# Performance work log

Measured on AMD Instinct MI355X. Metric: run time of the kernel, lower is better.

Reference implementation:

```python
import jax, jax.numpy as jnp
import numpy as np

B, S, D = 2, 2048, 4096
H, KV, HD = 32, 8, 128
ROPE_BASE = 10000.0


def rotate_half(x):
    x1, x2 = jnp.split(x, 2, axis=-1)
    return jnp.concatenate((-x2, x1), axis=-1)


def rope_tables(seq_len, head_dim, position_ids):
    inv_freq = 1.0 / (ROPE_BASE ** (jnp.arange(0, head_dim, 2, dtype=jnp.float32) / head_dim))
    t = jnp.arange(seq_len, dtype=jnp.float32)
    freqs = t[:, None] * inv_freq[None, :]            # [S, HD/2]
    emb = jnp.concatenate((freqs, freqs), axis=-1)     # [S, HD]
    cos = jnp.cos(emb)[position_ids][:, None]          # [B, 1, S, HD]
    sin = jnp.sin(emb)[position_ids][:, None]
    return cos, sin


def setup_inputs() -> dict:
    key = jax.random.key(0)
    ks = jax.random.split(key, 5)
    sc = 0.02
    return {
        "hidden_states": jax.random.normal(ks[0], (B, S, D), jnp.float32),
        "Wq": jax.random.normal(ks[1], (H * HD, D), jnp.float32) * sc,
        "Wk": jax.random.normal(ks[2], (KV * HD, D), jnp.float32) * sc,
        "Wv": jax.random.normal(ks[3], (KV * HD, D), jnp.float32) * sc,
        "Wo": jax.random.normal(ks[4], (D, H * HD), jnp.float32) * sc,
        "position_ids": jnp.broadcast_to(jnp.arange(S, dtype=jnp.int32), (B, S)),
    }


def reference(hidden_states, Wq, Wk, Wv, Wo, position_ids):
    b, s, _ = hidden_states.shape
    n_rep = H // KV

    q = (hidden_states @ Wq.T).reshape(b, s, H, HD).transpose(0, 2, 1, 3)   # [B,H,S,HD]
    k = (hidden_states @ Wk.T).reshape(b, s, KV, HD).transpose(0, 2, 1, 3)  # [B,KV,S,HD]
    v = (hidden_states @ Wv.T).reshape(b, s, KV, HD).transpose(0, 2, 1, 3)

    cos, sin = rope_tables(s, HD, position_ids)
    q = q * cos + rotate_half(q) * sin
    k = k * cos + rotate_half(k) * sin

    # repeat_kv: [B,KV,S,HD] -> [B,H,S,HD]
    k = jnp.repeat(k, n_rep, axis=1)
    v = jnp.repeat(v, n_rep, axis=1)

    scores = jnp.einsum("bhqd,bhkd->bhqk", q, k) / jnp.sqrt(jnp.float32(HD))
    # causal additive mask (what the surrounding model always supplies)
    causal = jnp.tril(jnp.ones((s, s), dtype=bool))
    scores = jnp.where(causal[None, None], scores, jnp.finfo(jnp.float32).min)
    attn = jax.nn.softmax(scores.astype(jnp.float32), axis=-1).astype(q.dtype)

    out = jnp.einsum("bhqk,bhkd->bhqd", attn, v)        # [B,H,S,HD]
    out = out.transpose(0, 2, 1, 3).reshape(b, s, H * HD)
    return out @ Wo.T
```

## Files before the change

### kernel.cpp

```cpp
#include <hip/hip_runtime.h>
#include <stdint.h>
#include <math.h>

#define B_  2
#define S_  2048
#define D_  4096
#define H_  32
#define KV_ 8
#define HD_ 128
#define M_  (B_ * S_)

typedef unsigned short u16;
typedef unsigned int   u32;

__device__ __forceinline__ float bf2f(u16 u) {
  union { u32 i; float f; } x; x.i = ((u32)u) << 16; return x.f;
}
__device__ __forceinline__ u16 f2bf(float f) {
  union { float f; u32 i; } x; x.f = f;
  u32 r = x.i + 0x7fffu + ((x.i >> 16) & 1u);
  return (u16)(r >> 16);
}
__device__ __forceinline__ u32 pack_bf16_rh(float hi, float lo) {
  union { float f; u32 i; } a, c; a.f = hi; c.f = lo;
  return __builtin_amdgcn_perm(a.i + 0x8000u, c.i + 0x8000u, 0x07060302u);
}

typedef __attribute__((ext_vector_type(8))) short bf16x8;
typedef __attribute__((ext_vector_type(4))) float f32x4;

__device__ __forceinline__ void async_cp16(const void* g, void* l) {
  __builtin_amdgcn_global_load_lds(
      (const __attribute__((address_space(1))) u32*)g,
      (__attribute__((address_space(3))) u32*)l, 16, 0, 0);
}

#define SBAR   asm volatile("s_barrier" ::: "memory")
#define WAITL0 asm volatile("s_waitcnt lgkmcnt(0)" ::: "memory")
#define WAITV(n) asm volatile("s_waitcnt vmcnt(" #n ")" ::: "memory")

__global__ void k_f32_to_bf16(const float* __restrict__ src, u16* __restrict__ dst, int n) {
  int i = (blockIdx.x * 256 + threadIdx.x) * 4;
  if (i >= n) return;
  float4 v = *(const float4*)(src + i);
  ushort4 o;
  o.x = f2bf(v.x); o.y = f2bf(v.y); o.z = f2bf(v.z); o.w = f2bf(v.w);
  *(ushort4*)(dst + i) = o;
}

template <typename OutT>
__global__ __launch_bounds__(512, 2) void k_gemm256_bt(const u16* __restrict__ A,
                                                       const u16* __restrict__ Bm,
                                                       OutT* __restrict__ C,
                                                       int M, int N, int K) {
  __shared__ __align__(16) u16 As[2][256 * 64];
  __shared__ __align__(16) u16 Bs[2][256 * 64];
  const int t = threadIdx.x;
  const int l = t & 63;
  const int w = t >> 6;
  const int wr = w >> 2, wc = w & 3;
  const int quad = l >> 4, lm = l & 15, l7 = l & 7;
  const int m0 = blockIdx.y * 256, n0 = blockIdx.x * 256;

  const int srow = t >> 3;
  const int scb  = (t & 7) ^ (srow & 7);
  const u16* srcA = A  + (size_t)(m0 + srow) * K + scb * 8;
  const u16* srcB = Bm + (size_t)(n0 + srow) * K + scb * 8;
  u16* dA = &As[0][0] + t * 8;
  u16* dB = &Bs[0][0] + t * 8;
  const size_t row64 = (size_t)64 * K;

  const int rowA = (wr * 128 + lm) * 64;
  const int rowB = (wc * 64 + lm) * 64;
  const int kq0 = ((0 * 4 + quad) ^ l7) * 8;
  const int kq1 = ((1 * 4 + quad) ^ l7) * 8;
  const u16* As0 = &As[0][0];
  const u16* Bs0 = &Bs[0][0];

  f32x4 acc[8][4];
#pragma unroll
  for (int i2 = 0; i2 < 8; ++i2)
#pragma unroll
    for (int j2 = 0; j2 < 4; ++j2) {
      f32x4 z = {0.f, 0.f, 0.f, 0.f};
      acc[i2][j2] = z;
    }

  auto stgA = [&](int buf, int kt, int h) {
    const u16* s = srcA + (size_t)kt * 64 + (size_t)(h * 128) * K;
    u16* d = dA + buf * 16384 + h * 8192;
    async_cp16(s, d);
    async_cp16(s + row64, d + 4096);
  };
  auto stgB = [&](int buf, int kt, int h) {
    const u16* s = srcB + (size_t)kt * 64 + (size_t)(h * 128) * K;
    u16* d = dB + buf * 16384 + h * 8192;
    async_cp16(s, d);
    async_cp16(s + row64, d + 4096);
  };

  stgA(0, 0, 0); stgA(0, 0, 1);
  stgB(0, 0, 0); stgB(0, 0, 1);
  stgB(1, 1, 0); stgB(1, 1, 1);
  WAITV(4);
  SBAR;

  const int iters = K >> 7;
  for (int i = 0; i < iters; ++i) {
    const int kt = 2 * i;
    const bool notLast = (i + 1 < iters);
#pragma unroll
    for (int hf = 0; hf < 2; ++hf) {
      bf16x8 bfr[4][2];
#pragma unroll
      for (int q = 0; q < 4; ++q) {
        if (q == 0) {
#pragma unroll
          for (int fn = 0; fn < 4; ++fn) {
            const int ro = hf * 16384 + rowB + fn * 1024;
            bfr[fn][0] = *(const bf16x8*)&Bs0[ro + kq0];
            bfr[fn][1] = *(const bf16x8*)&Bs0[ro + kq1];
          }
        }
        bf16x8 af[2][2];
#pragma unroll
        for (int fo = 0; fo < 2; ++fo) {
          const int ro = hf * 16384 + rowA + (2 * q + fo) * 1024;
          af[fo][0] = *(const bf16x8*)&As0[ro + kq0];
          af[fo][1] = *(const bf16x8*)&As0[ro + kq1];
        }
        if (hf == 0) {
          if (q == 0)      stgA(1, kt + 1, 0);
          else if (q == 1) stgA(1, kt + 1, 1);
          else if (q == 2) { if (notLast) stgB(0, kt + 2, 0); }
          else {
            if (notLast) { stgB(0, kt + 2, 1); WAITV(4); }
            else WAITV(0);
          }
        } else if (notLast) {
          if (q == 0)      stgA(0, kt + 2, 0);
          else if (q == 1) stgA(0, kt + 2, 1);
          else if (q == 2) stgB(1, kt + 3, 0);
          else { stgB(1, kt + 3, 1); WAITV(4); }
        }
        SBAR;
        WAITL0;
        __builtin_amdgcn_s_setprio(1);
#pragma unroll
        for (int fo = 0; fo < 2; ++fo)
#pragma unroll
          for (int fn = 0; fn < 4; ++fn)
            acc[2 * q + fo][fn] = __builtin_amdgcn_mfma_f32_16x16x32_bf16(
                af[fo][0], bfr[fn][0], acc[2 * q + fo][fn], 0, 0, 0);
#pragma unroll
        for (int fo = 0; fo < 2; ++fo)
#pragma unroll
          for (int fn = 0; fn < 4; ++fn)
            acc[2 * q + fo][fn] = __builtin_amdgcn_mfma_f32_16x16x32_bf16(
                af[fo][1], bfr[fn][1], acc[2 * q + fo][fn], 0, 0, 0);
        __builtin_amdgcn_s_setprio(0);
        SBAR;
      }
    }
  }

#pragma unroll
  for (int fm = 0; fm < 8; ++fm) {
    const int row = m0 + wr * 128 + fm * 16 + quad * 4;
#pragma unroll
    for (int fn = 0; fn < 4; ++fn) {
      const int col = n0 + wc * 64 + fn * 16 + lm;
#pragma unroll
      for (int r = 0; r < 4; ++r) {
        float v = acc[fm][fn][r];
        if constexpr (sizeof(OutT) == 2)
          C[(size_t)(row + r) * N + col] = (OutT)f2bf(v);
        else
          C[(size_t)(row + r) * N + col] = v;
      }
    }
  }
}

__global__ __launch_bounds__(256) void k_rope(u16* __restrict__ Q, u16* __restrict__ Km,
                                              const int* __restrict__ pos_ids) {
  const int t = threadIdx.x;
  const int bs = blockIdx.x * 4 + (t >> 6);
  const int d = t & 63;
  const int hg = blockIdx.y;
  const float pos = (float)pos_ids[bs];
  const float ang = pos * expf(-(float)d * 0.1439115683121279f);
  float sn, cs;
  sincosf(ang, &sn, &cs);
#pragma unroll
  for (int j = 0; j < 4; j++) {
    const int hh = hg * 4 + j;
    u16* p = (hh < H_) ? (Q + (size_t)bs * (H_ * HD_) + hh * HD_)
                       : (Km + (size_t)bs * 2048 + (hh - H_) * HD_);
    const float x1 = bf2f(p[d]);
    const float x2 = bf2f(p[d + 64]);
    p[d]      = f2bf(x1 * cs - x2 * sn);
    p[d + 64] = f2bf(x2 * cs + x1 * sn);
  }
}

__global__ __launch_bounds__(256) void k_transpose_v(const u16* __restrict__ KVb,
                                                     u16* __restrict__ Vt) {
  __shared__ u16 tile[64][136];
  const int s0 = blockIdx.x * 64;
  const int kvh = blockIdx.y & 7, b = blockIdx.y >> 3;
  const int t = threadIdx.x;
  const int sl = t >> 2, d0 = (t & 3) * 32;
  const u16* src = KVb + (size_t)(b * S_ + s0 + sl) * 2048 + 1024 + kvh * 128 + d0;
#pragma unroll
  for (int j = 0; j < 4; j++)
    *(uint4*)&tile[sl][d0 + j * 8] = *(const uint4*)(src + j * 8);
  __syncthreads();
  const int lt = t & 63, wv = t >> 6;
  u16* dst = Vt + ((size_t)(b * KV_ + kvh) * HD_) * (size_t)S_ + s0 + lt;
#pragma unroll
  for (int i = 0; i < 32; i++) {
    const int d = i * 4 + wv;
    dst[(size_t)d * S_] = tile[lt][d];
  }
}

__global__ __launch_bounds__(256, 2) void k_attn_mfma(const u16* __restrict__ Q,
                                                      const u16* __restrict__ KVb,
                                                      const u16* __restrict__ Vt,
                                                      u16* __restrict__ O) {
  __shared__ __align__(16) u16 Ks[2][64 * 128];
  __shared__ __align__(16) u16 Vs[2][128 * 64];
  __shared__ __align__(16) u16 Ps[128 * 64];
  const int qt = (S_ / 128 - 1) - blockIdx.x;
  const int h = blockIdx.y, b = blockIdx.z;
  const int kvh = h >> 2;
  const int t = threadIdx.x;
  const int w = t >> 6, l = t & 63;
  const int quad = l >> 4, lm = l & 15, l7 = l & 7;
  const int q0 = qt * 128, wq = w * 32;

  bf16x8 qf[2][4];
#pragma unroll
  for (int nt = 0; nt < 2; nt++)
#pragma unroll
    for (int ks = 0; ks < 4; ks++) {
      const int qrow = q0 + wq + nt * 16 + lm;
      qf[nt][ks] = *(const bf16x8*)(Q + (size_t)(b * S_ + qrow) * (H_ * HD_)
                                    + h * HD_ + ks * 32 + quad * 8);
    }

  const u16* kSrc[4]; const u16* vSrc[4];
  int dstOff[4];
#pragma unroll
  for (int j = 0; j < 4; j++) {
    const int c = w * 4 + j;
    kSrc[j] = KVb + (size_t)(b * S_ + c * 4 + (l >> 4)) * 2048 + kvh * 128
              + 8 * ((l & 15) ^ ((c & 1) * 4 + (l >> 4)));
    vSrc[j] = Vt + ((size_t)(b * KV_ + kvh) * HD_ + c * 8 + (l >> 3)) * (size_t)S_
              + 8 * ((l & 7) ^ (l >> 3));
    dstOff[j] = c * 512 + l * 8;
  }

  f32x4 Oa[8][2];
#pragma unroll
  for (int dt = 0; dt < 8; dt++)
#pragma unroll
    for (int nt = 0; nt < 2; nt++) {
      f32x4 z = {0.f, 0.f, 0.f, 0.f};
      Oa[dt][nt] = z;
    }
  float lsum[2] = {0.f, 0.f};

  const int nTiles = (qt + 1) * 2;

#pragma unroll
  for (int j = 0; j < 4; j++) {
    async_cp16(kSrc[j], &Ks[0][dstOff[j]]);
    async_cp16(vSrc[j], &Vs[0][dstOff[j]]);
  }

  for (int tile = 0; tile < nTiles; tile++) {
    const int cur = tile & 1;
    __builtin_amdgcn_s_waitcnt(0);
    __syncthreads();
    if (tile + 1 < nTiles) {
      const size_t kAdv = (size_t)(tile + 1) * 64 * 2048;
      const int vAdv = (tile + 1) * 64;
      const int nxt = cur ^ 1;
#pragma unroll
      for (int j = 0; j < 4; j++) {
        async_cp16(kSrc[j] + kAdv, &Ks[nxt][dstOff[j]]);
        async_cp16(vSrc[j] + vAdv, &Vs[nxt][dstOff[j]]);
      }
    }
    const u16* KsC = Ks[cur];
    const u16* VsC = Vs[cur];

    f32x4 st[4][2];
#pragma unroll
    for (int kvt = 0; kvt < 4; kvt++)
#pragma unroll
      for (int nt = 0; nt < 2; nt++) {
        f32x4 z = {0.f, 0.f, 0.f, 0.f};
        st[kvt][nt] = z;
      }
#pragma unroll
    for (int ks = 0; ks < 4; ks++) {
      bf16x8 kf[4];
#pragma unroll
      for (int kvt = 0; kvt < 4; kvt++)
        kf[kvt] = *(const bf16x8*)&KsC[(kvt * 16 + lm) * 128 + ((ks * 4 + quad) ^ l7) * 8];
#pragma unroll
      for (int kvt = 0; kvt < 4; kvt++) {
        st[kvt][0] = __builtin_amdgcn_mfma_f32_16x16x32_bf16(kf[kvt], qf[0][ks], st[kvt][0], 0, 0, 0);
        st[kvt][1] = __builtin_amdgcn_mfma_f32_16x16x32_bf16(kf[kvt], qf[1][ks], st[kvt][1], 0, 0, 0);
      }
    }

    const int kt0 = tile * 64;
    const bool diag = (tile >= nTiles - 2);
#pragma unroll
    for (int nt = 0; nt < 2; nt++) {
      const int qg = q0 + wq + nt * 16 + lm;
      const int prow = (wq + nt * 16 + lm) * 64;
#pragma unroll
      for (int kvt = 0; kvt < 4; kvt++) {
        float p[4];
#pragma unroll
        for (int r = 0; r < 4; r++) {
          float e = __expf(st[kvt][nt][r] * 0.08838834764831845f);
          if (diag) {
            const int kg = kt0 + kvt * 16 + quad * 4 + r;
            e = (kg <= qg) ? e : 0.f;
          }
          p[r] = e;
          lsum[nt] += e;
        }
        uint2 pk;
        pk.x = pack_bf16_rh(p[1], p[0]);
        pk.y = pack_bf16_rh(p[3], p[2]);
        const int pb = (2 * kvt + (quad >> 1)) ^ l7;
        *(uint2*)&Ps[prow + pb * 8 + (quad & 1) * 4] = pk;
      }
    }

#pragma unroll
    for (int ks2 = 0; ks2 < 2; ks2++) {
      const int pboff = ((ks2 * 4 + quad) ^ l7) * 8;
      bf16x8 pf0 = *(const bf16x8*)&Ps[(wq + lm) * 64 + pboff];
      bf16x8 pf1 = *(const bf16x8*)&Ps[(wq + 16 + lm) * 64 + pboff];
#pragma unroll
      for (int dt = 0; dt < 8; dt++) {
        bf16x8 vf = *(const bf16x8*)&VsC[(dt * 16 + lm) * 64 + pboff];
        Oa[dt][0] = __builtin_amdgcn_mfma_f32_16x16x32_bf16(vf, pf0, Oa[dt][0], 0, 0, 0);
        Oa[dt][1] = __builtin_amdgcn_mfma_f32_16x16x32_bf16(vf, pf1, Oa[dt][1], 0, 0, 0);
      }
    }
  }

#pragma unroll
  for (int nt = 0; nt < 2; nt++) {
    lsum[nt] += __shfl_xor(lsum[nt], 16);
    lsum[nt] += __shfl_xor(lsum[nt], 32);
  }
#pragma unroll
  for (int nt = 0; nt < 2; nt++) {
    const float inv = 1.f / lsum[nt];
    const int qg = q0 + wq + nt * 16 + lm;
    u16* obase = O + (size_t)(b * S_ + qg) * (H_ * HD_) + h * HD_ + quad * 4;
#pragma unroll
    for (int dt = 0; dt < 8; dt++) {
      uint2 pk;
      pk.x = pack_bf16_rh(Oa[dt][nt][1] * inv, Oa[dt][nt][0] * inv);
      pk.y = pack_bf16_rh(Oa[dt][nt][3] * inv, Oa[dt][nt][2] * inv);
      *(uint2*)(obase + dt * 16) = pk;
    }
  }
}

extern "C" void kernel_launch(void* const* d_in, const int* in_sizes, int n_in,
                              void* d_out, int out_size, void* d_ws, size_t ws_size,
                              hipStream_t stream) {
  const float* hs = (const float*)d_in[0];
  const float* Wq = (const float*)d_in[1];
  const float* Wk = (const float*)d_in[2];
  const float* Wv = (const float*)d_in[3];
  const float* Wo = (const float*)d_in[4];
  const int*  pos = (const int*)d_in[5];
  float* out = (float*)d_out;

  u16* hbuf = (u16*)d_ws;
  u16* wbuf = hbuf + (size_t)M_ * D_;
  u16* wkvb = wbuf + (size_t)(H_ * HD_) * D_;
  u16* Qb   = wkvb + (size_t)2048 * D_;
  u16* KVb  = Qb   + (size_t)M_ * (H_ * HD_);
  u16* Vt   = wkvb;

  const int nHid = M_ * D_;
  const int nWq  = H_ * HD_ * D_;
  const int nWk  = KV_ * HD_ * D_;

  k_f32_to_bf16<<<nHid / 1024, 256, 0, stream>>>(hs, hbuf, nHid);
  k_f32_to_bf16<<<nWq  / 1024, 256, 0, stream>>>(Wq, wbuf, nWq);
  k_f32_to_bf16<<<nWk  / 1024, 256, 0, stream>>>(Wk, wkvb, nWk);
  k_f32_to_bf16<<<nWk  / 1024, 256, 0, stream>>>(Wv, wkvb + (size_t)1024 * D_, nWk);

  dim3 blk(512);
  k_gemm256_bt<u16><<<dim3((H_ * HD_) / 256, M_ / 256), blk, 0, stream>>>(hbuf, wbuf, Qb,  M_, H_ * HD_, D_);
  k_gemm256_bt<u16><<<dim3(2048 / 256, M_ / 256),       blk, 0, stream>>>(hbuf, wkvb, KVb, M_, 2048,     D_);

  k_f32_to_bf16<<<nWq / 1024, 256, 0, stream>>>(Wo, wbuf, nWq);

  k_rope<<<dim3(M_ / 4, (H_ + KV_) / 4), 256, 0, stream>>>(Qb, KVb, pos);

  k_transpose_v<<<dim3(S_ / 64, B_ * KV_), 256, 0, stream>>>(KVb, Vt);

  k_attn_mfma<<<dim3(S_ / 128, H_, B_), 256, 0, stream>>>(Qb, KVb, Vt, hbuf);

  k_gemm256_bt<float><<<dim3(D_ / 256, M_ / 256), blk, 0, stream>>>(hbuf, wbuf, out, M_, D_, H_ * HD_);
}
```

Measured before the change: 770.8 us.

## Swizzle GEMM block order, keep P in registers, single-buffer V in attention

```diff
diff --git a/kernel.cpp b/kernel.cpp
--- a/kernel.cpp
+++ b/kernel.cpp
@@ -60,7 +60,13 @@
   const int w = t >> 6;
   const int wr = w >> 2, wc = w & 3;
   const int quad = l >> 4, lm = l & 15, l7 = l & 7;
-  const int m0 = blockIdx.y * 256, n0 = blockIdx.x * 256;
+
+  const u32 gx = gridDim.x, gy = gridDim.y;
+  const u32 bid = blockIdx.y * gx + blockIdx.x;
+  const u32 q8 = (gx * gy) >> 3;
+  const u32 cidx = (bid & 7u) * q8 + (bid >> 3);
+  const int m0 = (int)(cidx % gy) * 256;
+  const int n0 = (int)(cidx / gy) * 256;
 
   const int srow = t >> 3;
   const int scb  = (t & 7) ^ (srow & 7);
@@ -225,13 +231,12 @@
   }
 }
 
-__global__ __launch_bounds__(256, 2) void k_attn_mfma(const u16* __restrict__ Q,
+__global__ __launch_bounds__(256, 3) void k_attn_mfma(const u16* __restrict__ Q,
                                                       const u16* __restrict__ KVb,
                                                       const u16* __restrict__ Vt,
                                                       u16* __restrict__ O) {
   __shared__ __align__(16) u16 Ks[2][64 * 128];
-  __shared__ __align__(16) u16 Vs[2][128 * 64];
-  __shared__ __align__(16) u16 Ps[128 * 64];
+  __shared__ __align__(16) u16 Vs[128 * 64];
   const int qt = (S_ / 128 - 1) - blockIdx.x;
   const int h = blockIdx.y, b = blockIdx.z;
   const int kvh = h >> 2;
@@ -250,17 +255,16 @@
                                     + h * HD_ + ks * 32 + quad * 8);
     }
 
-  const u16* kSrc[4]; const u16* vSrc[4];
-  int dstOff[4];
-#pragma unroll
-  for (int j = 0; j < 4; j++) {
+  const u16* kSrc[2];
+#pragma unroll
+  for (int j = 0; j < 2; j++) {
     const int c = w * 4 + j;
     kSrc[j] = KVb + (size_t)(b * S_ + c * 4 + (l >> 4)) * 2048 + kvh * 128
               + 8 * ((l & 15) ^ ((c & 1) * 4 + (l >> 4)));
-    vSrc[j] = Vt + ((size_t)(b * KV_ + kvh) * HD_ + c * 8 + (l >> 3)) * (size_t)S_
-              + 8 * ((l & 7) ^ (l >> 3));
-    dstOff[j] = c * 512 + l * 8;
-  }
+  }
+  const u16* vSrc0 = Vt + ((size_t)(b * KV_ + kvh) * HD_ + (w * 4) * 8 + (l >> 3)) * (size_t)S_
+                     + 8 * ((l & 7) ^ (l >> 3));
+  const int dstOff0 = w * 2048 + l * 8;
 
   f32x4 Oa[8][2];
 #pragma unroll
@@ -273,29 +277,32 @@
   float lsum[2] = {0.f, 0.f};
 
   const int nTiles = (qt + 1) * 2;
-
-#pragma unroll
-  for (int j = 0; j < 4; j++) {
-    async_cp16(kSrc[j], &Ks[0][dstOff[j]]);
-    async_cp16(vSrc[j], &Vs[0][dstOff[j]]);
-  }
+  const int srcA = (quad & 1) * 32 + lm;
+  const int srcB = srcA + 16;
+  const bool hiKvt = (quad & 2) != 0;
+
+#pragma unroll
+  for (int j = 0; j < 4; j++)
+    async_cp16(kSrc[j & 1] + (j >> 1) * 16384, &Ks[0][dstOff0 + j * 512]);
 
   for (int tile = 0; tile < nTiles; tile++) {
     const int cur = tile & 1;
-    __builtin_amdgcn_s_waitcnt(0);
-    __syncthreads();
+    WAITV(0);
+    SBAR;
+    {
+      const size_t vAdv = (size_t)tile * 64;
+#pragma unroll
+      for (int j = 0; j < 4; j++)
+        async_cp16(vSrc0 + (size_t)j * 8 * S_ + vAdv, &Vs[dstOff0 + j * 512]);
+    }
     if (tile + 1 < nTiles) {
       const size_t kAdv = (size_t)(tile + 1) * 64 * 2048;
-      const int vAdv = (tile + 1) * 64;
       const int nxt = cur ^ 1;
 #pragma unroll
-      for (int j = 0; j < 4; j++) {
-        async_cp16(kSrc[j] + kAdv, &Ks[nxt][dstOff[j]]);
-        async_cp16(vSrc[j] + vAdv, &Vs[nxt][dstOff[j]]);
-      }
+      for (int j = 0; j < 4; j++)
+        async_cp16(kSrc[j & 1] + (j >> 1) * 16384 + kAdv, &Ks[nxt][dstOff0 + j * 512]);
     }
     const u16* KsC = Ks[cur];
-    const u16* VsC = Vs[cur];
 
     f32x4 st[4][2];
 #pragma unroll
@@ -311,19 +318,21 @@
 #pragma unroll
       for (int kvt = 0; kvt < 4; kvt++)
         kf[kvt] = *(const bf16x8*)&KsC[(kvt * 16 + lm) * 128 + ((ks * 4 + quad) ^ l7) * 8];
+      __builtin_amdgcn_s_setprio(1);
 #pragma unroll
       for (int kvt = 0; kvt < 4; kvt++) {
         st[kvt][0] = __builtin_amdgcn_mfma_f32_16x16x32_bf16(kf[kvt], qf[0][ks], st[kvt][0], 0, 0, 0);
         st[kvt][1] = __builtin_amdgcn_mfma_f32_16x16x32_bf16(kf[kvt], qf[1][ks], st[kvt][1], 0, 0, 0);
       }
+      __builtin_amdgcn_s_setprio(0);
     }
 
     const int kt0 = tile * 64;
     const bool diag = (tile >= nTiles - 2);
+    uint2 pkk[4][2];
 #pragma unroll
     for (int nt = 0; nt < 2; nt++) {
       const int qg = q0 + wq + nt * 16 + lm;
-      const int prow = (wq + nt * 16 + lm) * 64;
 #pragma unroll
       for (int kvt = 0; kvt < 4; kvt++) {
         float p[4];
@@ -337,25 +346,44 @@
           p[r] = e;
           lsum[nt] += e;
         }
-        uint2 pk;
-        pk.x = pack_bf16_rh(p[1], p[0]);
-        pk.y = pack_bf16_rh(p[3], p[2]);
-        const int pb = (2 * kvt + (quad >> 1)) ^ l7;
-        *(uint2*)&Ps[prow + pb * 8 + (quad & 1) * 4] = pk;
-      }
-    }
+        pkk[kvt][nt].x = pack_bf16_rh(p[1], p[0]);
+        pkk[kvt][nt].y = pack_bf16_rh(p[3], p[2]);
+      }
+    }
+
+    if (tile + 1 < nTiles) { WAITV(4); }
+    else                   { WAITV(0); }
+    SBAR;
 
 #pragma unroll
     for (int ks2 = 0; ks2 < 2; ks2++) {
-      const int pboff = ((ks2 * 4 + quad) ^ l7) * 8;
-      bf16x8 pf0 = *(const bf16x8*)&Ps[(wq + lm) * 64 + pboff];
-      bf16x8 pf1 = *(const bf16x8*)&Ps[(wq + 16 + lm) * 64 + pboff];
+      bf16x8 pf[2];
+#pragma unroll
+      for (int nt = 0; nt < 2; nt++) {
+        const u32 a0x = (u32)__shfl((int)pkk[2 * ks2][nt].x, srcA);
+        const u32 a0y = (u32)__shfl((int)pkk[2 * ks2][nt].y, srcA);
+        const u32 a1x = (u32)__shfl((int)pkk[2 * ks2 + 1][nt].x, srcA);
+        const u32 a1y = (u32)__shfl((int)pkk[2 * ks2 + 1][nt].y, srcA);
+        const u32 b0x = (u32)__shfl((int)pkk[2 * ks2][nt].x, srcB);
+        const u32 b0y = (u32)__shfl((int)pkk[2 * ks2][nt].y, srcB);
+        const u32 b1x = (u32)__shfl((int)pkk[2 * ks2 + 1][nt].x, srcB);
+        const u32 b1y = (u32)__shfl((int)pkk[2 * ks2 + 1][nt].y, srcB);
+        union { u32 u[4]; bf16x8 v; } pu;
+        pu.u[0] = hiKvt ? a1x : a0x;
+        pu.u[1] = hiKvt ? a1y : a0y;
+        pu.u[2] = hiKvt ? b1x : b0x;
+        pu.u[3] = hiKvt ? b1y : b0y;
+        pf[nt] = pu.v;
+      }
+      const int vboff = ((ks2 * 4 + quad) ^ l7) * 8;
+      __builtin_amdgcn_s_setprio(1);
 #pragma unroll
       for (int dt = 0; dt < 8; dt++) {
-        bf16x8 vf = *(const bf16x8*)&VsC[(dt * 16 + lm) * 64 + pboff];
-        Oa[dt][0] = __builtin_amdgcn_mfma_f32_16x16x32_bf16(vf, pf0, Oa[dt][0], 0, 0, 0);
-        Oa[dt][1] = __builtin_amdgcn_mfma_f32_16x16x32_bf16(vf, pf1, Oa[dt][1], 0, 0, 0);
-      }
+        bf16x8 vf = *(const bf16x8*)&Vs[(dt * 16 + lm) * 64 + vboff];
+        Oa[dt][0] = __builtin_amdgcn_mfma_f32_16x16x32_bf16(vf, pf[0], Oa[dt][0], 0, 0, 0);
+        Oa[dt][1] = __builtin_amdgcn_mfma_f32_16x16x32_bf16(vf, pf[1], Oa[dt][1], 0, 0, 0);
+      }
+      __builtin_amdgcn_s_setprio(0);
     }
   }
 
```

Result: slower. 836.0 us (+8.5%).
